# Performance work log

Hardware: AMD Instinct MI355X
Metric: run time of the kernel (lower is better)

The kernel has to match this reference:

```python
import jax, jax.numpy as jnp
import numpy as np

EMBED_DIM = 1024

def setup_inputs() -> dict:
    key = jax.random.key(0)
    kx, kq, kk, kv = jax.random.split(key, 4)
    scale = 1.0 / np.sqrt(EMBED_DIM)  # Kaiming-uniform-ish init scale
    x = jax.random.normal(kx, (4, 2048, EMBED_DIM), dtype=jnp.float32)
    Wq = jax.random.uniform(kq, (EMBED_DIM, EMBED_DIM), jnp.float32, -scale, scale)
    Wk = jax.random.uniform(kk, (EMBED_DIM, EMBED_DIM), jnp.float32, -scale, scale)
    Wv = jax.random.uniform(kv, (EMBED_DIM, EMBED_DIM), jnp.float32, -scale, scale)
    return {"x": x, "Wq": Wq, "Wk": Wk, "Wv": Wv}

def reference(x, Wq, Wk, Wv):
    # Linear layers: y = x @ W.T (torch nn.Linear convention, no bias)
    q = jnp.einsum('bsd,ed->bse', x, Wq)
    k = jnp.einsum('bsd,ed->bse', x, Wk)
    v = jnp.einsum('bsd,ed->bse', x, Wv)
    d = k.shape[-1]
    scores = jnp.einsum('bqe,bke->bqk', q, k) / jnp.sqrt(jnp.asarray(d, x.dtype))
    attn = jax.nn.softmax(scores, axis=-1)
    return jnp.einsum('bqk,bke->bqe', attn, v)
```

## Files before the change

kernel.cpp:

```cpp
#include <hip/hip_runtime.h>
#include <hip/hip_bf16.h>

typedef unsigned short u16;
typedef __bf16 bf16x8 __attribute__((ext_vector_type(8)));
typedef float f32x4 __attribute__((ext_vector_type(4)));

#define MEMF() asm volatile("" ::: "memory")

__device__ __forceinline__ u16 f2bf(float f) {
    unsigned int u = __builtin_bit_cast(unsigned int, f);
    unsigned int r = u + 0x7FFFu + ((u >> 16) & 1u);
    return (u16)(r >> 16);
}

__device__ __forceinline__ float bf2f(unsigned int bits16) {
    return __builtin_bit_cast(float, bits16 << 16);
}

__device__ __forceinline__ void gload_lds16(const u16* g, u16* l) {
    __builtin_amdgcn_global_load_lds(
        (const __attribute__((address_space(1))) void*)(g),
        (__attribute__((address_space(3))) void*)(l), 16, 0, 0);
}

__global__ __launch_bounds__(256) void cvt_bf16_kernel(
    const float* __restrict__ in, u16* __restrict__ out, int n8)
{
    int i = blockIdx.x * 256 + threadIdx.x;
    if (i >= n8) return;
    const float4* p = (const float4*)in + 2 * (long long)i;
    float4 a = p[0], b = p[1];
    uint4 o;
    o.x = (unsigned)f2bf(a.x) | ((unsigned)f2bf(a.y) << 16);
    o.y = (unsigned)f2bf(a.z) | ((unsigned)f2bf(a.w) << 16);
    o.z = (unsigned)f2bf(b.x) | ((unsigned)f2bf(b.y) << 16);
    o.w = (unsigned)f2bf(b.z) | ((unsigned)f2bf(b.w) << 16);
    ((uint4*)out)[i] = o;
}

template <int BN, bool OUT_F32>
__global__ __launch_bounds__(512, 2) void gemm2p(
    const u16* __restrict__ A, const u16* __restrict__ B, void* __restrict__ Cv,
    int lda, int ldb, int ldc, int K,
    long long sAz, long long sBz, long long sCz)
{
    constexpr int NF = BN / 64;
    constexpr int NH = NF / 2;
    constexpr int BLOADS = BN / 64;
    constexpr int BNK = BN * 64;

    extern __shared__ u16 lds[];
    u16* ldsB = lds + 32768;

    const int z = blockIdx.z;
    A += (long long)z * sAz;
    B += (long long)z * sBz;

    const int tid  = threadIdx.x;
    const int lane = tid & 63;
    const int wave = tid >> 6;
    const int wr = wave >> 2, wc = wave & 3;
    const int m0 = blockIdx.y << 8, n0 = blockIdx.x * BN;
    const int NT = K >> 6;

    const u16* gAp[4];
    const u16* gBp[BLOADS];
#pragma unroll
    for (int i = 0; i < 4; ++i) {
        int s = tid + i * 512, row = ((s >> 7) << 4) | (s & 15), g = (s >> 4) & 7;
        gAp[i] = A + (long long)(m0 + row) * lda + g * 8;
    }
#pragma unroll
    for (int i = 0; i < BLOADS; ++i) {
        int s = tid + i * 512, row = ((s >> 7) << 4) | (s & 15), g = (s >> 4) & 7;
        gBp[i] = B + (long long)(n0 + row) * ldb + g * 8;
    }

    auto stage = [&](int kt, int buf) {
#pragma unroll
        for (int i = 0; i < 4; ++i)
            gload_lds16(gAp[i] + (long long)kt * 64, lds + buf * 16384 + (tid + i * 512) * 8);
#pragma unroll
        for (int i = 0; i < BLOADS; ++i)
            gload_lds16(gBp[i] + (long long)kt * 64, ldsB + buf * BNK + (tid + i * 512) * 8);
    };

    f32x4 acc[8][NF] = {};

    stage(0, 0);
    stage(1, 1);
    if constexpr (BN == 256) asm volatile("s_waitcnt vmcnt(8)" ::: "memory");
    else                     asm volatile("s_waitcnt vmcnt(6)" ::: "memory");
    __builtin_amdgcn_s_barrier();
    MEMF();

    for (int kt = 0; kt < NT; ++kt) {
        const int cur = kt & 1;
        const u16* sAc = lds  + cur * 16384 + lane * 8;
        const u16* sBc = ldsB + cur * BNK   + lane * 8;

        bf16x8 a_[4][2], b0[NH][2], b1[NH][2];
#pragma unroll
        for (int mi = 0; mi < 4; ++mi)
#pragma unroll
            for (int kk = 0; kk < 2; ++kk)
                a_[mi][kk] = *(const bf16x8*)(sAc + ((wr * 8 + mi) * 8 + kk * 4) * 128);
#pragma unroll
        for (int ni = 0; ni < NH; ++ni)
#pragma unroll
            for (int kk = 0; kk < 2; ++kk) {
                b0[ni][kk] = *(const bf16x8*)(sBc + ((wc * NF + ni) * 8 + kk * 4) * 128);
                b1[ni][kk] = *(const bf16x8*)(sBc + ((wc * NF + NH + ni) * 8 + kk * 4) * 128);
            }
#pragma unroll
        for (int kk = 0; kk < 2; ++kk)
#pragma unroll
            for (int mi = 0; mi < 4; ++mi) {
#pragma unroll
                for (int ni = 0; ni < NH; ++ni)
                    acc[mi][ni] = __builtin_amdgcn_mfma_f32_16x16x32_bf16(
                        a_[mi][kk], b0[ni][kk], acc[mi][ni], 0, 0, 0);
#pragma unroll
                for (int ni = 0; ni < NH; ++ni)
                    acc[mi][NH + ni] = __builtin_amdgcn_mfma_f32_16x16x32_bf16(
                        a_[mi][kk], b1[ni][kk], acc[mi][NH + ni], 0, 0, 0);
            }
#pragma unroll
        for (int mi = 0; mi < 4; ++mi)
#pragma unroll
            for (int kk = 0; kk < 2; ++kk)
                a_[mi][kk] = *(const bf16x8*)(sAc + ((wr * 8 + 4 + mi) * 8 + kk * 4) * 128);
#pragma unroll
        for (int kk = 0; kk < 2; ++kk)
#pragma unroll
            for (int mi = 0; mi < 4; ++mi) {
#pragma unroll
                for (int ni = 0; ni < NH; ++ni)
                    acc[4 + mi][ni] = __builtin_amdgcn_mfma_f32_16x16x32_bf16(
                        a_[mi][kk], b0[ni][kk], acc[4 + mi][ni], 0, 0, 0);
#pragma unroll
                for (int ni = 0; ni < NH; ++ni)
                    acc[4 + mi][NH + ni] = __builtin_amdgcn_mfma_f32_16x16x32_bf16(
                        a_[mi][kk], b1[ni][kk], acc[4 + mi][NH + ni], 0, 0, 0);
            }

        MEMF();
        __builtin_amdgcn_s_barrier();
        if (kt + 2 < NT) {
            stage(kt + 2, cur);
            if constexpr (BN == 256) asm volatile("s_waitcnt vmcnt(8)" ::: "memory");
            else                     asm volatile("s_waitcnt vmcnt(6)" ::: "memory");
        } else {
            asm volatile("s_waitcnt vmcnt(0)" ::: "memory");
        }
        __builtin_amdgcn_s_barrier();
        MEMF();
    }

    const int fl = lane & 15, fg = lane >> 4;
    const int er0 = m0 + wr * 128 + fg * 4;
    const int ec0 = n0 + wc * (NF * 16) + fl;
    if constexpr (OUT_F32) {
        float* C = (float*)Cv + (long long)z * sCz;
#pragma unroll
        for (int mi = 0; mi < 8; ++mi)
#pragma unroll
            for (int ni = 0; ni < NF; ++ni)
#pragma unroll
                for (int j = 0; j < 4; ++j)
                    C[(long long)(er0 + mi * 16 + j) * ldc + ec0 + ni * 16] = acc[mi][ni][j];
    } else {
        u16* C = (u16*)Cv + (long long)z * sCz;
#pragma unroll
        for (int mi = 0; mi < 8; ++mi)
#pragma unroll
            for (int ni = 0; ni < NF; ++ni)
#pragma unroll
                for (int j = 0; j < 4; ++j)
                    C[(long long)(er0 + mi * 16 + j) * ldc + ec0 + ni * 16] = f2bf(acc[mi][ni][j]);
    }
}

__global__ __launch_bounds__(256) void softmax_rows(u16* __restrict__ S)
{
    const long long row = blockIdx.x;
    u16* p = S + row * 2048;
    const int tid = threadIdx.x;
    const int lane = tid & 63, wave = tid >> 6;

    uint4 r4 = ((const uint4*)p)[tid];
    unsigned u[4] = {r4.x, r4.y, r4.z, r4.w};
    float v[8];
    const float scale = 1.0f / 32.0f;
#pragma unroll
    for (int i = 0; i < 4; ++i) {
        v[2 * i]     = bf2f(u[i] & 0xFFFFu) * scale;
        v[2 * i + 1] = __builtin_bit_cast(float, u[i] & 0xFFFF0000u) * scale;
    }
    float mx = v[0];
#pragma unroll
    for (int i = 1; i < 8; ++i) mx = fmaxf(mx, v[i]);
#pragma unroll
    for (int off = 32; off >= 1; off >>= 1) mx = fmaxf(mx, __shfl_xor(mx, off, 64));

    __shared__ float redmax[4], redsum[4];
    if (lane == 0) redmax[wave] = mx;
    __syncthreads();
    mx = fmaxf(fmaxf(redmax[0], redmax[1]), fmaxf(redmax[2], redmax[3]));

    float s = 0.f;
#pragma unroll
    for (int i = 0; i < 8; ++i) { v[i] = __expf(v[i] - mx); s += v[i]; }
#pragma unroll
    for (int off = 32; off >= 1; off >>= 1) s += __shfl_xor(s, off, 64);
    if (lane == 0) redsum[wave] = s;
    __syncthreads();
    s = redsum[0] + redsum[1] + redsum[2] + redsum[3];
    float inv = 1.0f / s;

    uint4 o;
    unsigned ov[4];
#pragma unroll
    for (int i = 0; i < 4; ++i)
        ov[i] = (unsigned)f2bf(v[2 * i] * inv) |
                ((unsigned)f2bf(v[2 * i + 1] * inv) << 16);
    o.x = ov[0]; o.y = ov[1]; o.z = ov[2]; o.w = ov[3];
    ((uint4*)p)[tid] = o;
}

extern "C" void kernel_launch(void* const* d_in, const int* in_sizes, int n_in,
                              void* d_out, int out_size, void* d_ws, size_t ws_size,
                              hipStream_t stream) {
    const float* x  = (const float*)d_in[0];
    const float* Wq = (const float*)d_in[1];
    const float* Wk = (const float*)d_in[2];
    const float* Wv = (const float*)d_in[3];
    float* out = (float*)d_out;

    const int B = 4, S = 2048, D = 1024;
    const long long MS = (long long)B * S;

    u16* Sc  = (u16*)d_ws;
    u16* xb  = Sc;
    u16* wqk = Sc  + (long long)B * S * S;
    u16* wvb = wqk + 2 * D * D;
    u16* qk  = wvb + D * D;
    u16* vT  = qk  + MS * 2 * D;
    size_t need = (size_t)2 * ((long long)B * S * S + 3 * D * D + MS * 2 * D + MS * D);
    if (ws_size < need) return;

    hipFuncSetAttribute(reinterpret_cast<const void*>(&gemm2p<256, false>),
                        hipFuncAttributeMaxDynamicSharedMemorySize, 131072);
    hipFuncSetAttribute(reinterpret_cast<const void*>(&gemm2p<128, false>),
                        hipFuncAttributeMaxDynamicSharedMemorySize, 98304);
    hipFuncSetAttribute(reinterpret_cast<const void*>(&gemm2p<128, true>),
                        hipFuncAttributeMaxDynamicSharedMemorySize, 98304);

    cvt_bf16_kernel<<<(int)(MS * D / 8 / 256), 256, 0, stream>>>(x, xb, (int)(MS * D / 8));
    cvt_bf16_kernel<<<D * D / 8 / 256, 256, 0, stream>>>(Wq, wqk, D * D / 8);
    cvt_bf16_kernel<<<D * D / 8 / 256, 256, 0, stream>>>(Wk, wqk + D * D, D * D / 8);
    cvt_bf16_kernel<<<D * D / 8 / 256, 256, 0, stream>>>(Wv, wvb, D * D / 8);

    gemm2p<256, false><<<dim3(2 * D / 256, (int)(MS / 256), 1), 512, 131072, stream>>>(
        xb, wqk, qk, D, D, 2 * D, D, 0, 0, 0);

    gemm2p<128, false><<<dim3((int)(MS / 128), D / 256, 1), 512, 98304, stream>>>(
        wvb, xb, vT, D, D, (int)MS, D, 0, 0, 0);

    gemm2p<256, false><<<dim3(S / 256, S / 256, B), 512, 131072, stream>>>(
        qk, qk + D, Sc, 2 * D, 2 * D, S, D,
        (long long)S * 2 * D, (long long)S * 2 * D, (long long)S * S);

    softmax_rows<<<(int)(B * S), 256, 0, stream>>>(Sc);

    gemm2p<128, true><<<dim3(D / 128, S / 256, B), 512, 98304, stream>>>(
        Sc, vT, out, S, (int)MS, D, S,
        (long long)S * S, (long long)S, (long long)S * D);
}
```

Baseline: 197.1 us.

## Split GEMM K-step into four barrier-separated phases with interleaved prefetch and XCD-aware tile remap

```diff
diff --git a/kernel.cpp b/kernel.cpp
--- a/kernel.cpp
+++ b/kernel.cpp
@@ -39,18 +39,26 @@
 }
 
 template <int BN, bool OUT_F32>
-__global__ __launch_bounds__(512, 2) void gemm2p(
+__global__ __launch_bounds__(512, 2) void gemm4p(
     const u16* __restrict__ A, const u16* __restrict__ B, void* __restrict__ Cv,
     int lda, int ldb, int ldc, int K,
-    long long sAz, long long sBz, long long sCz)
+    long long sAz, long long sBz, long long sCz, int cw, int ch)
 {
-    constexpr int NF = BN / 64;
-    constexpr int NH = NF / 2;
+    constexpr int WC = (BN == 256) ? 4 : 2;
+    constexpr int ROWS = (BN == 256) ? 128 : 64;
+    constexpr int MI = ROWS / 16;
+    constexpr int MIh = MI / 2;
     constexpr int BLOADS = BN / 64;
     constexpr int BNK = BN * 64;
 
     extern __shared__ u16 lds[];
     u16* ldsB = lds + 32768;
+
+    const int flat = blockIdx.x + gridDim.x * blockIdx.y;
+    const int xcd = flat & 7, jj = flat >> 3;
+    const int nCx = gridDim.x / cw;
+    const int bx = (xcd % nCx) * cw + jj % cw;
+    const int by = (xcd / nCx) * ch + jj / cw;
 
     const int z = blockIdx.z;
     A += (long long)z * sAz;
@@ -59,8 +67,8 @@
     const int tid  = threadIdx.x;
     const int lane = tid & 63;
     const int wave = tid >> 6;
-    const int wr = wave >> 2, wc = wave & 3;
-    const int m0 = blockIdx.y << 8, n0 = blockIdx.x * BN;
+    const int wr = wave / WC, wc = wave % WC;
+    const int m0 = by << 8, n0 = bx * BN;
     const int NT = K >> 6;
 
     const u16* gAp[4];
@@ -75,20 +83,23 @@
         int s = tid + i * 512, row = ((s >> 7) << 4) | (s & 15), g = (s >> 4) & 7;
         gBp[i] = B + (long long)(n0 + row) * ldb + g * 8;
     }
-
-    auto stage = [&](int kt, int buf) {
-#pragma unroll
-        for (int i = 0; i < 4; ++i)
-            gload_lds16(gAp[i] + (long long)kt * 64, lds + buf * 16384 + (tid + i * 512) * 8);
-#pragma unroll
-        for (int i = 0; i < BLOADS; ++i)
-            gload_lds16(gBp[i] + (long long)kt * 64, ldsB + buf * BNK + (tid + i * 512) * 8);
+    auto stA = [&](int kt, int buf, int i) {
+        gload_lds16(gAp[i] + (long long)kt * 64, lds + buf * 16384 + (tid + i * 512) * 8);
     };
-
-    f32x4 acc[8][NF] = {};
-
-    stage(0, 0);
-    stage(1, 1);
+    auto stB = [&](int kt, int buf, int i) {
+        gload_lds16(gBp[i] + (long long)kt * 64, ldsB + buf * BNK + (tid + i * 512) * 8);
+    };
+
+    f32x4 acc[MI][4] = {};
+
+#pragma unroll
+    for (int i = 0; i < 4; ++i) stA(0, 0, i);
+#pragma unroll
+    for (int i = 0; i < BLOADS; ++i) stB(0, 0, i);
+#pragma unroll
+    for (int i = 0; i < 4; ++i) stA(1, 1, i);
+#pragma unroll
+    for (int i = 0; i < BLOADS; ++i) stB(1, 1, i);
     if constexpr (BN == 256) asm volatile("s_waitcnt vmcnt(8)" ::: "memory");
     else                     asm volatile("s_waitcnt vmcnt(6)" ::: "memory");
     __builtin_amdgcn_s_barrier();
@@ -98,83 +109,127 @@
         const int cur = kt & 1;
         const u16* sAc = lds  + cur * 16384 + lane * 8;
         const u16* sBc = ldsB + cur * BNK   + lane * 8;
-
-        bf16x8 a_[4][2], b0[NH][2], b1[NH][2];
-#pragma unroll
-        for (int mi = 0; mi < 4; ++mi)
+        const bool st = (kt + 2 < NT);
+
+        bf16x8 a[MIh][2], b0[2][2], b1[2][2];
+
+#pragma unroll
+        for (int mi = 0; mi < MIh; ++mi)
 #pragma unroll
             for (int kk = 0; kk < 2; ++kk)
-                a_[mi][kk] = *(const bf16x8*)(sAc + ((wr * 8 + mi) * 8 + kk * 4) * 128);
-#pragma unroll
-        for (int ni = 0; ni < NH; ++ni)
-#pragma unroll
-            for (int kk = 0; kk < 2; ++kk) {
-                b0[ni][kk] = *(const bf16x8*)(sBc + ((wc * NF + ni) * 8 + kk * 4) * 128);
-                b1[ni][kk] = *(const bf16x8*)(sBc + ((wc * NF + NH + ni) * 8 + kk * 4) * 128);
+                a[mi][kk] = *(const bf16x8*)(sAc + ((wr * MI + mi) * 8 + kk * 4) * 128);
+#pragma unroll
+        for (int ni = 0; ni < 2; ++ni)
+#pragma unroll
+            for (int kk = 0; kk < 2; ++kk)
+                b0[ni][kk] = *(const bf16x8*)(sBc + ((wc * 4 + ni) * 8 + kk * 4) * 128);
+        MEMF(); __builtin_amdgcn_s_barrier();
+        asm volatile("s_waitcnt lgkmcnt(0)" ::: "memory");
+        __builtin_amdgcn_s_setprio(1);
+#pragma unroll
+        for (int kk = 0; kk < 2; ++kk)
+#pragma unroll
+            for (int mi = 0; mi < MIh; ++mi)
+#pragma unroll
+                for (int ni = 0; ni < 2; ++ni)
+                    acc[mi][ni] = __builtin_amdgcn_mfma_f32_16x16x32_bf16(
+                        a[mi][kk], b0[ni][kk], acc[mi][ni], 0, 0, 0);
+        __builtin_amdgcn_s_setprio(0);
+        MEMF(); __builtin_amdgcn_s_barrier();
+
+#pragma unroll
+        for (int ni = 0; ni < 2; ++ni)
+#pragma unroll
+            for (int kk = 0; kk < 2; ++kk)
+                b1[ni][kk] = *(const bf16x8*)(sBc + ((wc * 4 + 2 + ni) * 8 + kk * 4) * 128);
+        if constexpr (BN == 256) {
+            if (st) { stA(kt + 2, cur, 0); stA(kt + 2, cur, 2); }
+        }
+        MEMF(); __builtin_amdgcn_s_barrier();
+        asm volatile("s_waitcnt lgkmcnt(0)" ::: "memory");
+        __builtin_amdgcn_s_setprio(1);
+#pragma unroll
+        for (int kk = 0; kk < 2; ++kk)
+#pragma unroll
+            for (int mi = 0; mi < MIh; ++mi)
+#pragma unroll
+                for (int ni = 0; ni < 2; ++ni)
+                    acc[mi][2 + ni] = __builtin_amdgcn_mfma_f32_16x16x32_bf16(
+                        a[mi][kk], b1[ni][kk], acc[mi][2 + ni], 0, 0, 0);
+        __builtin_amdgcn_s_setprio(0);
+        MEMF(); __builtin_amdgcn_s_barrier();
+
+#pragma unroll
+        for (int mi = 0; mi < MIh; ++mi)
+#pragma unroll
+            for (int kk = 0; kk < 2; ++kk)
+                a[mi][kk] = *(const bf16x8*)(sAc + ((wr * MI + MIh + mi) * 8 + kk * 4) * 128);
+        if (st) {
+            if constexpr (BN == 256) { stB(kt + 2, cur, 0); stB(kt + 2, cur, 1); }
+            else                     { stB(kt + 2, cur, 0); }
+        }
+        MEMF(); __builtin_amdgcn_s_barrier();
+        asm volatile("s_waitcnt lgkmcnt(0)" ::: "memory");
+        __builtin_amdgcn_s_setprio(1);
+#pragma unroll
+        for (int kk = 0; kk < 2; ++kk)
+#pragma unroll
+            for (int mi = 0; mi < MIh; ++mi)
+#pragma unroll
+                for (int ni = 0; ni < 2; ++ni)
+                    acc[MIh + mi][ni] = __builtin_amdgcn_mfma_f32_16x16x32_bf16(
+                        a[mi][kk], b0[ni][kk], acc[MIh + mi][ni], 0, 0, 0);
+        __builtin_amdgcn_s_setprio(0);
+        MEMF(); __builtin_amdgcn_s_barrier();
+
+        if (st) {
+            if constexpr (BN == 256) {
+                stA(kt + 2, cur, 1); stA(kt + 2, cur, 3);
+                stB(kt + 2, cur, 2); stB(kt + 2, cur, 3);
+            } else {
+                stA(kt + 2, cur, 0); stA(kt + 2, cur, 1);
+                stA(kt + 2, cur, 2); stA(kt + 2, cur, 3);
+                stB(kt + 2, cur, 1);
             }
+        }
+        MEMF(); __builtin_amdgcn_s_barrier();
+        __builtin_amdgcn_s_setprio(1);
 #pragma unroll
         for (int kk = 0; kk < 2; ++kk)
 #pragma unroll
-            for (int mi = 0; mi < 4; ++mi) {
-#pragma unroll
-                for (int ni = 0; ni < NH; ++ni)
-                    acc[mi][ni] = __builtin_amdgcn_mfma_f32_16x16x32_bf16(
-                        a_[mi][kk], b0[ni][kk], acc[mi][ni], 0, 0, 0);
-#pragma unroll
-                for (int ni = 0; ni < NH; ++ni)
-                    acc[mi][NH + ni] = __builtin_amdgcn_mfma_f32_16x16x32_bf16(
-                        a_[mi][kk], b1[ni][kk], acc[mi][NH + ni], 0, 0, 0);
-            }
-#pragma unroll
-        for (int mi = 0; mi < 4; ++mi)
-#pragma unroll
-            for (int kk = 0; kk < 2; ++kk)
-                a_[mi][kk] = *(const bf16x8*)(sAc + ((wr * 8 + 4 + mi) * 8 + kk * 4) * 128);
-#pragma unroll
-        for (int kk = 0; kk < 2; ++kk)
-#pragma unroll
-            for (int mi = 0; mi < 4; ++mi) {
-#pragma unroll
-                for (int ni = 0; ni < NH; ++ni)
-                    acc[4 + mi][ni] = __builtin_amdgcn_mfma_f32_16x16x32_bf16(
-                        a_[mi][kk], b0[ni][kk], acc[4 + mi][ni], 0, 0, 0);
-#pragma unroll
-                for (int ni = 0; ni < NH; ++ni)
-                    acc[4 + mi][NH + ni] = __builtin_amdgcn_mfma_f32_16x16x32_bf16(
-                        a_[mi][kk], b1[ni][kk], acc[4 + mi][NH + ni], 0, 0, 0);
-            }
-
-        MEMF();
-        __builtin_amdgcn_s_barrier();
-        if (kt + 2 < NT) {
-            stage(kt + 2, cur);
+            for (int mi = 0; mi < MIh; ++mi)
+#pragma unroll
+                for (int ni = 0; ni < 2; ++ni)
+                    acc[MIh + mi][2 + ni] = __builtin_amdgcn_mfma_f32_16x16x32_bf16(
+                        a[mi][kk], b1[ni][kk], acc[MIh + mi][2 + ni], 0, 0, 0);
+        __builtin_amdgcn_s_setprio(0);
+        if (st) {
             if constexpr (BN == 256) asm volatile("s_waitcnt vmcnt(8)" ::: "memory");
             else                     asm volatile("s_waitcnt vmcnt(6)" ::: "memory");
-        } else {
+        } else if (kt + 1 < NT) {
             asm volatile("s_waitcnt vmcnt(0)" ::: "memory");
         }
-        __builtin_amdgcn_s_barrier();
-        MEMF();
+        MEMF(); __builtin_amdgcn_s_barrier();
     }
 
     const int fl = lane & 15, fg = lane >> 4;
-    const int er0 = m0 + wr * 128 + fg * 4;
-    const int ec0 = n0 + wc * (NF * 16) + fl;
+    const int er0 = m0 + wr * ROWS + fg * 4;
+    const int ec0 = n0 + wc * 64 + fl;
     if constexpr (OUT_F32) {
         float* C = (float*)Cv + (long long)z * sCz;
 #pragma unroll
-        for (int mi = 0; mi < 8; ++mi)
-#pragma unroll
-            for (int ni = 0; ni < NF; ++ni)
+        for (int mi = 0; mi < MI; ++mi)
+#pragma unroll
+            for (int ni = 0; ni < 4; ++ni)
 #pragma unroll
                 for (int j = 0; j < 4; ++j)
                     C[(long long)(er0 + mi * 16 + j) * ldc + ec0 + ni * 16] = acc[mi][ni][j];
     } else {
         u16* C = (u16*)Cv + (long long)z * sCz;
 #pragma unroll
-        for (int mi = 0; mi < 8; ++mi)
-#pragma unroll
-            for (int ni = 0; ni < NF; ++ni)
+        for (int mi = 0; mi < MI; ++mi)
+#pragma unroll
+            for (int ni = 0; ni < 4; ++ni)
 #pragma unroll
                 for (int j = 0; j < 4; ++j)
                     C[(long long)(er0 + mi * 16 + j) * ldc + ec0 + ni * 16] = f2bf(acc[mi][ni][j]);
@@ -249,11 +304,11 @@
     size_t need = (size_t)2 * ((long long)B * S * S + 3 * D * D + MS * 2 * D + MS * D);
     if (ws_size < need) return;
 
-    hipFuncSetAttribute(reinterpret_cast<const void*>(&gemm2p<256, false>),
+    hipFuncSetAttribute(reinterpret_cast<const void*>(&gemm4p<256, false>),
                         hipFuncAttributeMaxDynamicSharedMemorySize, 131072);
-    hipFuncSetAttribute(reinterpret_cast<const void*>(&gemm2p<128, false>),
+    hipFuncSetAttribute(reinterpret_cast<const void*>(&gemm4p<128, false>),
                         hipFuncAttributeMaxDynamicSharedMemorySize, 98304);
-    hipFuncSetAttribute(reinterpret_cast<const void*>(&gemm2p<128, true>),
+    hipFuncSetAttribute(reinterpret_cast<const void*>(&gemm4p<128, true>),
                         hipFuncAttributeMaxDynamicSharedMemorySize, 98304);
 
     cvt_bf16_kernel<<<(int)(MS * D / 8 / 256), 256, 0, stream>>>(x, xb, (int)(MS * D / 8));
@@ -261,19 +316,19 @@
     cvt_bf16_kernel<<<D * D / 8 / 256, 256, 0, stream>>>(Wk, wqk + D * D, D * D / 8);
     cvt_bf16_kernel<<<D * D / 8 / 256, 256, 0, stream>>>(Wv, wvb, D * D / 8);
 
-    gemm2p<256, false><<<dim3(2 * D / 256, (int)(MS / 256), 1), 512, 131072, stream>>>(
-        xb, wqk, qk, D, D, 2 * D, D, 0, 0, 0);
-
-    gemm2p<128, false><<<dim3((int)(MS / 128), D / 256, 1), 512, 98304, stream>>>(
-        wvb, xb, vT, D, D, (int)MS, D, 0, 0, 0);
-
-    gemm2p<256, false><<<dim3(S / 256, S / 256, B), 512, 131072, stream>>>(
+    gemm4p<256, false><<<dim3(2 * D / 256, (int)(MS / 256), 1), 512, 131072, stream>>>(
+        xb, wqk, qk, D, D, 2 * D, D, 0, 0, 0, 8, 4);
+
+    gemm4p<128, false><<<dim3((int)(MS / 128), D / 256, 1), 512, 98304, stream>>>(
+        wvb, xb, vT, D, D, (int)MS, D, 0, 0, 0, 8, 4);
+
+    gemm4p<256, false><<<dim3(S / 256, S / 256, B), 512, 131072, stream>>>(
         qk, qk + D, Sc, 2 * D, 2 * D, S, D,
-        (long long)S * 2 * D, (long long)S * 2 * D, (long long)S * S);
+        (long long)S * 2 * D, (long long)S * 2 * D, (long long)S * S, 2, 4);
 
     softmax_rows<<<(int)(B * S), 256, 0, stream>>>(Sc);
 
-    gemm2p<128, true><<<dim3(D / 128, S / 256, B), 512, 98304, stream>>>(
+    gemm4p<128, true><<<dim3(D / 128, S / 256, B), 512, 98304, stream>>>(
         Sc, vT, out, S, (int)MS, D, S,
-        (long long)S * S, (long long)S, (long long)S * D);
-}
+        (long long)S * S, (long long)S, (long long)S * D, 4, 2);
+}
```

Measured after the change: 195.3 us. About the same (-0.9%).

## Replace 256-wide GEMM with 128x128 tile kernel using XCD-aware block swizzle

Applied to the files above, without the earlier changes.

```diff
diff --git a/kernel.cpp b/kernel.cpp
--- a/kernel.cpp
+++ b/kernel.cpp
@@ -38,119 +38,80 @@
     ((uint4*)out)[i] = o;
 }
 
-template <int BN, bool OUT_F32>
-__global__ __launch_bounds__(512, 2) void gemm2p(
+template <bool OUT_F32>
+__global__ __launch_bounds__(256) void gemm97(
     const u16* __restrict__ A, const u16* __restrict__ B, void* __restrict__ Cv,
     int lda, int ldb, int ldc, int K,
-    long long sAz, long long sBz, long long sCz)
+    long long sAz, long long sBz, long long sCz, int cw, int ch)
 {
-    constexpr int NF = BN / 64;
-    constexpr int NH = NF / 2;
-    constexpr int BLOADS = BN / 64;
-    constexpr int BNK = BN * 64;
-
-    extern __shared__ u16 lds[];
-    u16* ldsB = lds + 32768;
+    __shared__ u16 lds[4 * 4096];
+    u16* ldsB = lds + 8192;
+
+    const int flat = blockIdx.x + gridDim.x * blockIdx.y;
+    const int xcd = flat & 7, jj = flat >> 3;
+    const int nCx = gridDim.x / cw;
+    const int bx = (xcd % nCx) * cw + jj % cw;
+    const int by = (xcd / nCx) * ch + jj / cw;
 
     const int z = blockIdx.z;
     A += (long long)z * sAz;
     B += (long long)z * sBz;
 
-    const int tid  = threadIdx.x;
-    const int lane = tid & 63;
-    const int wave = tid >> 6;
-    const int wr = wave >> 2, wc = wave & 3;
-    const int m0 = blockIdx.y << 8, n0 = blockIdx.x * BN;
-    const int NT = K >> 6;
-
-    const u16* gAp[4];
-    const u16* gBp[BLOADS];
-#pragma unroll
-    for (int i = 0; i < 4; ++i) {
-        int s = tid + i * 512, row = ((s >> 7) << 4) | (s & 15), g = (s >> 4) & 7;
-        gAp[i] = A + (long long)(m0 + row) * lda + g * 8;
-    }
-#pragma unroll
-    for (int i = 0; i < BLOADS; ++i) {
-        int s = tid + i * 512, row = ((s >> 7) << 4) | (s & 15), g = (s >> 4) & 7;
-        gBp[i] = B + (long long)(n0 + row) * ldb + g * 8;
-    }
-
+    const int tid = threadIdx.x, lane = tid & 63, wave = tid >> 6;
+    const int wr = wave >> 1, wc = wave & 1;
+    const int m0 = by << 7, n0 = bx << 7;
+    const int NT = K >> 5;
+
+    const u16* gA[2];
+    const u16* gB[2];
+#pragma unroll
+    for (int i = 0; i < 2; ++i) {
+        int s = tid + i * 256;
+        int row = ((s >> 6) << 4) | (s & 15), g = (s >> 4) & 3;
+        gA[i] = A + (long long)(m0 + row) * lda + g * 8;
+        gB[i] = B + (long long)(n0 + row) * ldb + g * 8;
+    }
     auto stage = [&](int kt, int buf) {
 #pragma unroll
-        for (int i = 0; i < 4; ++i)
-            gload_lds16(gAp[i] + (long long)kt * 64, lds + buf * 16384 + (tid + i * 512) * 8);
-#pragma unroll
-        for (int i = 0; i < BLOADS; ++i)
-            gload_lds16(gBp[i] + (long long)kt * 64, ldsB + buf * BNK + (tid + i * 512) * 8);
+        for (int i = 0; i < 2; ++i) {
+            gload_lds16(gA[i] + (long long)kt * 32, lds  + buf * 4096 + (tid + i * 256) * 8);
+            gload_lds16(gB[i] + (long long)kt * 32, ldsB + buf * 4096 + (tid + i * 256) * 8);
+        }
     };
 
-    f32x4 acc[8][NF] = {};
+    f32x4 acc[4][4] = {};
 
     stage(0, 0);
     stage(1, 1);
-    if constexpr (BN == 256) asm volatile("s_waitcnt vmcnt(8)" ::: "memory");
-    else                     asm volatile("s_waitcnt vmcnt(6)" ::: "memory");
+    asm volatile("s_waitcnt vmcnt(4)" ::: "memory");
     __builtin_amdgcn_s_barrier();
     MEMF();
 
     for (int kt = 0; kt < NT; ++kt) {
         const int cur = kt & 1;
-        const u16* sAc = lds  + cur * 16384 + lane * 8;
-        const u16* sBc = ldsB + cur * BNK   + lane * 8;
-
-        bf16x8 a_[4][2], b0[NH][2], b1[NH][2];
-#pragma unroll
-        for (int mi = 0; mi < 4; ++mi)
-#pragma unroll
-            for (int kk = 0; kk < 2; ++kk)
-                a_[mi][kk] = *(const bf16x8*)(sAc + ((wr * 8 + mi) * 8 + kk * 4) * 128);
-#pragma unroll
-        for (int ni = 0; ni < NH; ++ni)
-#pragma unroll
-            for (int kk = 0; kk < 2; ++kk) {
-                b0[ni][kk] = *(const bf16x8*)(sBc + ((wc * NF + ni) * 8 + kk * 4) * 128);
-                b1[ni][kk] = *(const bf16x8*)(sBc + ((wc * NF + NH + ni) * 8 + kk * 4) * 128);
-            }
-#pragma unroll
-        for (int kk = 0; kk < 2; ++kk)
-#pragma unroll
-            for (int mi = 0; mi < 4; ++mi) {
-#pragma unroll
-                for (int ni = 0; ni < NH; ++ni)
-                    acc[mi][ni] = __builtin_amdgcn_mfma_f32_16x16x32_bf16(
-                        a_[mi][kk], b0[ni][kk], acc[mi][ni], 0, 0, 0);
-#pragma unroll
-                for (int ni = 0; ni < NH; ++ni)
-                    acc[mi][NH + ni] = __builtin_amdgcn_mfma_f32_16x16x32_bf16(
-                        a_[mi][kk], b1[ni][kk], acc[mi][NH + ni], 0, 0, 0);
-            }
-#pragma unroll
-        for (int mi = 0; mi < 4; ++mi)
-#pragma unroll
-            for (int kk = 0; kk < 2; ++kk)
-                a_[mi][kk] = *(const bf16x8*)(sAc + ((wr * 8 + 4 + mi) * 8 + kk * 4) * 128);
-#pragma unroll
-        for (int kk = 0; kk < 2; ++kk)
-#pragma unroll
-            for (int mi = 0; mi < 4; ++mi) {
-#pragma unroll
-                for (int ni = 0; ni < NH; ++ni)
-                    acc[4 + mi][ni] = __builtin_amdgcn_mfma_f32_16x16x32_bf16(
-                        a_[mi][kk], b0[ni][kk], acc[4 + mi][ni], 0, 0, 0);
-#pragma unroll
-                for (int ni = 0; ni < NH; ++ni)
-                    acc[4 + mi][NH + ni] = __builtin_amdgcn_mfma_f32_16x16x32_bf16(
-                        a_[mi][kk], b1[ni][kk], acc[4 + mi][NH + ni], 0, 0, 0);
-            }
+        const u16* sAc = lds  + cur * 4096 + lane * 8;
+        const u16* sBc = ldsB + cur * 4096 + lane * 8;
+
+        bf16x8 a[4], b[4];
+#pragma unroll
+        for (int mi = 0; mi < 4; ++mi)
+            a[mi] = *(const bf16x8*)(sAc + (wr * 4 + mi) * 512);
+#pragma unroll
+        for (int ni = 0; ni < 4; ++ni)
+            b[ni] = *(const bf16x8*)(sBc + (wc * 4 + ni) * 512);
+#pragma unroll
+        for (int mi = 0; mi < 4; ++mi)
+#pragma unroll
+            for (int ni = 0; ni < 4; ++ni)
+                acc[mi][ni] = __builtin_amdgcn_mfma_f32_16x16x32_bf16(
+                    a[mi], b[ni], acc[mi][ni], 0, 0, 0);
 
         MEMF();
         __builtin_amdgcn_s_barrier();
         if (kt + 2 < NT) {
             stage(kt + 2, cur);
-            if constexpr (BN == 256) asm volatile("s_waitcnt vmcnt(8)" ::: "memory");
-            else                     asm volatile("s_waitcnt vmcnt(6)" ::: "memory");
-        } else {
+            asm volatile("s_waitcnt vmcnt(4)" ::: "memory");
+        } else if (kt + 1 < NT) {
             asm volatile("s_waitcnt vmcnt(0)" ::: "memory");
         }
         __builtin_amdgcn_s_barrier();
@@ -158,23 +119,23 @@
     }
 
     const int fl = lane & 15, fg = lane >> 4;
-    const int er0 = m0 + wr * 128 + fg * 4;
-    const int ec0 = n0 + wc * (NF * 16) + fl;
+    const int er0 = m0 + wr * 64 + fg * 4;
+    const int ec0 = n0 + wc * 64 + fl;
     if constexpr (OUT_F32) {
         float* C = (float*)Cv + (long long)z * sCz;
 #pragma unroll
-        for (int mi = 0; mi < 8; ++mi)
-#pragma unroll
-            for (int ni = 0; ni < NF; ++ni)
+        for (int mi = 0; mi < 4; ++mi)
+#pragma unroll
+            for (int ni = 0; ni < 4; ++ni)
 #pragma unroll
                 for (int j = 0; j < 4; ++j)
                     C[(long long)(er0 + mi * 16 + j) * ldc + ec0 + ni * 16] = acc[mi][ni][j];
     } else {
         u16* C = (u16*)Cv + (long long)z * sCz;
 #pragma unroll
-        for (int mi = 0; mi < 8; ++mi)
-#pragma unroll
-            for (int ni = 0; ni < NF; ++ni)
+        for (int mi = 0; mi < 4; ++mi)
+#pragma unroll
+            for (int ni = 0; ni < 4; ++ni)
 #pragma unroll
                 for (int j = 0; j < 4; ++j)
                     C[(long long)(er0 + mi * 16 + j) * ldc + ec0 + ni * 16] = f2bf(acc[mi][ni][j]);
@@ -249,31 +210,24 @@
     size_t need = (size_t)2 * ((long long)B * S * S + 3 * D * D + MS * 2 * D + MS * D);
     if (ws_size < need) return;
 
-    hipFuncSetAttribute(reinterpret_cast<const void*>(&gemm2p<256, false>),
-                        hipFuncAttributeMaxDynamicSharedMemorySize, 131072);
-    hipFuncSetAttribute(reinterpret_cast<const void*>(&gemm2p<128, false>),
-                        hipFuncAttributeMaxDynamicSharedMemorySize, 98304);
-    hipFuncSetAttribute(reinterpret_cast<const void*>(&gemm2p<128, true>),
-                        hipFuncAttributeMaxDynamicSharedMemorySize, 98304);
-
     cvt_bf16_kernel<<<(int)(MS * D / 8 / 256), 256, 0, stream>>>(x, xb, (int)(MS * D / 8));
     cvt_bf16_kernel<<<D * D / 8 / 256, 256, 0, stream>>>(Wq, wqk, D * D / 8);
     cvt_bf16_kernel<<<D * D / 8 / 256, 256, 0, stream>>>(Wk, wqk + D * D, D * D / 8);
     cvt_bf16_kernel<<<D * D / 8 / 256, 256, 0, stream>>>(Wv, wvb, D * D / 8);
 
-    gemm2p<256, false><<<dim3(2 * D / 256, (int)(MS / 256), 1), 512, 131072, stream>>>(
-        xb, wqk, qk, D, D, 2 * D, D, 0, 0, 0);
-
-    gemm2p<128, false><<<dim3((int)(MS / 128), D / 256, 1), 512, 98304, stream>>>(
-        wvb, xb, vT, D, D, (int)MS, D, 0, 0, 0);
-
-    gemm2p<256, false><<<dim3(S / 256, S / 256, B), 512, 131072, stream>>>(
+    gemm97<false><<<dim3(2 * D / 128, (int)(MS / 128), 1), 256, 0, stream>>>(
+        xb, wqk, qk, D, D, 2 * D, D, 0, 0, 0, 8, 16);
+
+    gemm97<false><<<dim3((int)(MS / 128), D / 128, 1), 256, 0, stream>>>(
+        wvb, xb, vT, D, D, (int)MS, D, 0, 0, 0, 8, 8);
+
+    gemm97<false><<<dim3(S / 128, S / 128, B), 256, 0, stream>>>(
         qk, qk + D, Sc, 2 * D, 2 * D, S, D,
-        (long long)S * 2 * D, (long long)S * 2 * D, (long long)S * S);
+        (long long)S * 2 * D, (long long)S * 2 * D, (long long)S * S, 4, 8);
 
     softmax_rows<<<(int)(B * S), 256, 0, stream>>>(Sc);
 
-    gemm2p<128, true><<<dim3(D / 128, S / 256, B), 512, 98304, stream>>>(
+    gemm97<true><<<dim3(D / 128, S / 128, B), 256, 0, stream>>>(
         Sc, vT, out, S, (int)MS, D, S,
-        (long long)S * S, (long long)S, (long long)S * D);
-}
+        (long long)S * S, (long long)S, (long long)S * D, 4, 4);
+}
```

Measured after the change: 259.2 us. 1.31x slower.
